# Performance work log

Measured on AMD Instinct MI355X. Metric: run time of the kernel, lower is better.

The kernel has to match this reference:

```python
import jax, jax.numpy as jnp
import numpy as np

INPUT_SIZE = 1024
HIDDEN_SIZE = 1024
BATCH = 32
SEQ_LEN = 1024


def setup_inputs() -> dict:
    key = jax.random.key(0)
    k1, k2, k3, k4 = jax.random.split(key, 4)
    scale_x = 1.0 / np.sqrt(INPUT_SIZE)
    scale_h = 1.0 / np.sqrt(HIDDEN_SIZE)
    X = jax.random.normal(k1, (BATCH, SEQ_LEN, INPUT_SIZE), dtype=jnp.float32)
    W_xh = jax.random.normal(k2, (INPUT_SIZE, HIDDEN_SIZE), dtype=jnp.float32) * scale_x
    W_hh = jax.random.normal(k3, (HIDDEN_SIZE, HIDDEN_SIZE), dtype=jnp.float32) * scale_h
    b_h = jax.random.normal(k4, (HIDDEN_SIZE,), dtype=jnp.float32) * 0.01
    return {"X": X, "W_xh": W_xh, "W_hh": W_hh, "b_h": b_h}


def reference(X, W_xh, W_hh, b_h):
    # Elman RNN: H_t = tanh(X_t @ W_xh + H_{t-1} @ W_hh + b)
    B, S, _ = X.shape
    H0 = jnp.zeros((B, W_hh.shape[0]), dtype=X.dtype)
    # Precompute input projection for all timesteps in one big GEMM.
    Xp = jnp.einsum('bsi,ih->bsh', X, W_xh) + b_h  # [B, S, H]

    def step(H, xp_t):
        H_new = jnp.tanh(xp_t + H @ W_hh)
        return H_new, H_new

    H_last, outs = jax.lax.scan(step, H0, jnp.swapaxes(Xp, 0, 1))  # outs: [S, B, H]
    out = jnp.swapaxes(outs, 0, 1)  # [B, S, H]
    return out, H_last
```

## Files before the change

kernel.cpp:

```cpp
#include <hip/hip_runtime.h>
#include <math.h>


#define B_SZ 32
#define S_SZ 1024
#define H_SZ 1024
#define K_SZ 1024

#define BM 128
#define BN 128
#define BK 8

__global__ __launch_bounds__(256) void proj_gemm(
    const float* __restrict__ A,
    const float* __restrict__ Bm,
    const float* __restrict__ bias,
    float* __restrict__ C,
    int M, int N, int K)
{
    __shared__ float As[BK][BM];
    __shared__ float Bs[BK][BN];

    const int tid  = threadIdx.x;
    const int row0 = blockIdx.y * BM;
    const int col0 = blockIdx.x * BN;
    const int tx = tid & 15;
    const int ty = tid >> 4;
    const int mBase = ty * 8;
    const int nBase = tx * 8;

    float acc[8][8];
    #pragma unroll
    for (int i = 0; i < 8; ++i)
        #pragma unroll
        for (int j = 0; j < 8; ++j) acc[i][j] = 0.f;

    for (int k0 = 0; k0 < K; k0 += BK) {
        {
            const int r  = tid >> 1;
            const int kq = (tid & 1) * 4;
            const float4 av = *(const float4*)(&A[(size_t)(row0 + r) * K + k0 + kq]);
            As[kq + 0][r] = av.x;
            As[kq + 1][r] = av.y;
            As[kq + 2][r] = av.z;
            As[kq + 3][r] = av.w;
            const int kr = tid >> 5;
            const int cq = (tid & 31) * 4;
            *(float4*)(&Bs[kr][cq]) =
                *(const float4*)(&Bm[(size_t)(k0 + kr) * N + col0 + cq]);
        }
        __syncthreads();

        #pragma unroll
        for (int kk = 0; kk < BK; ++kk) {
            float a[8], b[8];
            *(float4*)&a[0] = *(const float4*)&As[kk][mBase];
            *(float4*)&a[4] = *(const float4*)&As[kk][mBase + 4];
            *(float4*)&b[0] = *(const float4*)&Bs[kk][nBase];
            *(float4*)&b[4] = *(const float4*)&Bs[kk][nBase + 4];
            #pragma unroll
            for (int i = 0; i < 8; ++i)
                #pragma unroll
                for (int j = 0; j < 8; ++j)
                    acc[i][j] += a[i] * b[j];
        }
        __syncthreads();
    }

    #pragma unroll
    for (int i = 0; i < 8; ++i) {
        const int r = row0 + mBase + i;
        #pragma unroll
        for (int jq = 0; jq < 8; jq += 4) {
            const int c = col0 + nBase + jq;
            const float4 bv = *(const float4*)(&bias[c]);
            float4 o;
            o.x = acc[i][jq + 0] + bv.x;
            o.y = acc[i][jq + 1] + bv.y;
            o.z = acc[i][jq + 2] + bv.z;
            o.w = acc[i][jq + 3] + bv.w;
            *(float4*)(&C[(size_t)r * N + c]) = o;
        }
    }
}

__global__ void init_cnt(unsigned int* __restrict__ cnt, int n) {
    int i = blockIdx.x * 256 + threadIdx.x;
    if (i < n) cnt[i] = 0u;
}

__device__ __forceinline__ float fast_tanh(float x) {
    const float cx = fminf(fmaxf(x, -15.f), 15.f);
    const float e  = __expf(2.f * cx);
    return __fdividef(e - 1.f, e + 1.f);
}

__global__ __launch_bounds__(512, 2) void rnn_persist(
    float* __restrict__ HS,
    const float* __restrict__ W,
    float* __restrict__ Hlast,
    unsigned int* __restrict__ cnt
    )
{
    const int g    = blockIdx.x & 7;
    const int c    = blockIdx.x >> 3;
    const int col0 = c * 32;
    const int b0   = g * 4;
    const int tid  = threadIdx.x;
    const int j    = tid & 31;
    const int seg  = tid >> 5;

    __shared__ __align__(16) float Hs[4][1024];
    __shared__ float red[8][4][32];

    float w[64];
    {
        const float* wp = W + (size_t)(seg * 64) * H_SZ + col0 + j;
        #pragma unroll
        for (int i = 0; i < 64; ++i) w[i] = wp[(size_t)i * H_SZ];
        #pragma unroll
        for (int i = 0; i < 64; ++i) asm volatile("" : "+v"(w[i]));
    }

    unsigned int* flag = cnt + g * S_SZ;

    const int eb = tid >> 5;
    const int ej = tid & 31;

    for (int t = 0; t < S_SZ; ++t) {
        float xp = 0.f;
        size_t eidx = 0;
        if (tid < 128) {
            eidx = ((size_t)(b0 + eb) * S_SZ + t) * H_SZ + col0 + ej;
            xp = HS[eidx];
        }

        if (t > 0) {
            if (tid == 0) {
                while (__hip_atomic_load(flag + (t - 1), __ATOMIC_RELAXED,
                                         __HIP_MEMORY_SCOPE_AGENT) < 32u) {
                    __builtin_amdgcn_s_sleep(2);
                }
            }
            __syncthreads();

            #pragma unroll
            for (int ch = 0; ch < 4; ++ch) {
                const int f8 = tid + ch * 512;
                const int b  = f8 >> 9;
                const int qw = f8 & 511;
                const unsigned long long* src = (const unsigned long long*)
                    (&HS[((size_t)(b0 + b) * S_SZ + (t - 1)) * H_SZ]);
                const unsigned long long v8 = __hip_atomic_load(
                    &src[qw], __ATOMIC_RELAXED, __HIP_MEMORY_SCOPE_AGENT);
                *(unsigned long long*)(&Hs[b][qw * 2]) = v8;
            }
            __syncthreads();

            float acc[4];
            #pragma unroll
            for (int b = 0; b < 4; ++b) {
                const float4* hb = (const float4*)(&Hs[b][seg * 64]);
                float a = 0.f;
                #pragma unroll
                for (int q = 0; q < 16; ++q) {
                    const float4 h = hb[q];
                    a += h.x * w[4 * q + 0];
                    a += h.y * w[4 * q + 1];
                    a += h.z * w[4 * q + 2];
                    a += h.w * w[4 * q + 3];
                }
                acc[b] = a;
            }
            #pragma unroll
            for (int b = 0; b < 4; ++b) acc[b] += __shfl_xor(acc[b], 32);
            const int wv = tid >> 6;
            if ((tid & 63) < 32) {
                #pragma unroll
                for (int b = 0; b < 4; ++b) red[wv][b][j] = acc[b];
            }
            __syncthreads();
        }

        if (tid < 128) {
            float s = 0.f;
            if (t > 0) {
                #pragma unroll
                for (int wv2 = 0; wv2 < 8; ++wv2) s += red[wv2][eb][ej];
            }
            const float v = fast_tanh(xp + s);
            __hip_atomic_store(&HS[eidx], v, __ATOMIC_RELAXED,
                               __HIP_MEMORY_SCOPE_AGENT);
            if (t == S_SZ - 1)
                Hlast[(size_t)(b0 + eb) * H_SZ + col0 + ej] = v;
        }

        __syncthreads();
        if (tid == 0) {
            __hip_atomic_fetch_add(flag + t, 1u, __ATOMIC_RELAXED,
                                   __HIP_MEMORY_SCOPE_AGENT);
        }
    }
}

extern "C" void kernel_launch(void* const* d_in, const int* in_sizes, int n_in,
                              void* d_out, int out_size, void* d_ws, size_t ws_size,
                              hipStream_t stream) {
    const float* X    = (const float*)d_in[0];
    const float* W_xh = (const float*)d_in[1];
    const float* W_hh = (const float*)d_in[2];
    const float* b_h  = (const float*)d_in[3];
    float* out = (float*)d_out;
    float* Hlast = out + (size_t)B_SZ * S_SZ * H_SZ;
    unsigned int* cnt = (unsigned int*)d_ws;

    init_cnt<<<(8 * S_SZ + 255) / 256, 256, 0, stream>>>(cnt, 8 * S_SZ);

    dim3 gridA(H_SZ / BN, (B_SZ * S_SZ) / BM);
    proj_gemm<<<gridA, 256, 0, stream>>>(X, W_xh, b_h, out,
                                         B_SZ * S_SZ, H_SZ, K_SZ);

    rnn_persist<<<256, 512, 0, stream>>>(out, W_hh, Hlast, cnt);
}
```

Baseline: 4.248 ms.

## Replace counter flags with per-element tagged values in double-buffered exchange

Hidden-state values are published as 64-bit words packing the timestep tag with the float, in a two-slot parity buffer. Consumers poll each element directly until its tag matches, removing the single-thread flag spin, a block barrier and the per-step atomic counter increment. This cuts per-step synchronization latency on the sequential recurrence, at the cost of doubled exchange traffic and all threads spinning on global memory.

```diff
diff --git a/kernel.cpp b/kernel.cpp
--- a/kernel.cpp
+++ b/kernel.cpp
@@ -84,9 +84,9 @@
     }
 }
 
-__global__ void init_cnt(unsigned int* __restrict__ cnt, int n) {
+__global__ void init_hx(unsigned long long* __restrict__ hx, int n) {
     int i = blockIdx.x * 256 + threadIdx.x;
-    if (i < n) cnt[i] = 0u;
+    if (i < n) hx[i] = 0xFFFFFFFF00000000ULL;
 }
 
 __device__ __forceinline__ float fast_tanh(float x) {
@@ -99,7 +99,7 @@
     float* __restrict__ HS,
     const float* __restrict__ W,
     float* __restrict__ Hlast,
-    unsigned int* __restrict__ cnt
+    unsigned long long* __restrict__ Hx
     )
 {
     const int g    = blockIdx.x & 7;
@@ -122,7 +122,7 @@
         for (int i = 0; i < 64; ++i) asm volatile("" : "+v"(w[i]));
     }
 
-    unsigned int* flag = cnt + g * S_SZ;
+    const size_t PAR = (size_t)B_SZ * H_SZ;
 
     const int eb = tid >> 5;
     const int ej = tid & 31;
@@ -136,24 +136,30 @@
         }
 
         if (t > 0) {
-            if (tid == 0) {
-                while (__hip_atomic_load(flag + (t - 1), __ATOMIC_RELAXED,
-                                         __HIP_MEMORY_SCOPE_AGENT) < 32u) {
-                    __builtin_amdgcn_s_sleep(2);
+            const unsigned int want = (unsigned int)(t - 1);
+            const unsigned long long* hxr =
+                Hx + ((size_t)((t - 1) & 1)) * PAR + (size_t)b0 * H_SZ;
+
+            unsigned long long v[8];
+            #pragma unroll
+            for (int q = 0; q < 8; ++q) {
+                v[q] = __hip_atomic_load(hxr + tid + 512 * q,
+                                         __ATOMIC_RELAXED,
+                                         __HIP_MEMORY_SCOPE_AGENT);
+            }
+            #pragma unroll
+            for (int q = 0; q < 8; ++q) {
+                while ((unsigned int)(v[q] >> 32) != want) {
+                    v[q] = __hip_atomic_load(hxr + tid + 512 * q,
+                                             __ATOMIC_RELAXED,
+                                             __HIP_MEMORY_SCOPE_AGENT);
                 }
             }
-            __syncthreads();
-
-            #pragma unroll
-            for (int ch = 0; ch < 4; ++ch) {
-                const int f8 = tid + ch * 512;
-                const int b  = f8 >> 9;
-                const int qw = f8 & 511;
-                const unsigned long long* src = (const unsigned long long*)
-                    (&HS[((size_t)(b0 + b) * S_SZ + (t - 1)) * H_SZ]);
-                const unsigned long long v8 = __hip_atomic_load(
-                    &src[qw], __ATOMIC_RELAXED, __HIP_MEMORY_SCOPE_AGENT);
-                *(unsigned long long*)(&Hs[b][qw * 2]) = v8;
+            #pragma unroll
+            for (int q = 0; q < 8; ++q) {
+                const int e = tid + 512 * q;
+                Hs[e >> 10][e & 1023] =
+                    __uint_as_float((unsigned int)v[q]);
             }
             __syncthreads();
 
@@ -179,8 +185,8 @@
                 #pragma unroll
                 for (int b = 0; b < 4; ++b) red[wv][b][j] = acc[b];
             }
-            __syncthreads();
-        }
+        }
+        __syncthreads();
 
         if (tid < 128) {
             float s = 0.f;
@@ -189,16 +195,16 @@
                 for (int wv2 = 0; wv2 < 8; ++wv2) s += red[wv2][eb][ej];
             }
             const float v = fast_tanh(xp + s);
-            __hip_atomic_store(&HS[eidx], v, __ATOMIC_RELAXED,
-                               __HIP_MEMORY_SCOPE_AGENT);
+            HS[eidx] = v;
+            const unsigned long long pk =
+                ((unsigned long long)(unsigned int)t << 32) |
+                (unsigned long long)__float_as_uint(v);
+            __hip_atomic_store(
+                Hx + ((size_t)(t & 1)) * PAR +
+                    (size_t)(b0 + eb) * H_SZ + col0 + ej,
+                pk, __ATOMIC_RELAXED, __HIP_MEMORY_SCOPE_AGENT);
             if (t == S_SZ - 1)
                 Hlast[(size_t)(b0 + eb) * H_SZ + col0 + ej] = v;
-        }
-
-        __syncthreads();
-        if (tid == 0) {
-            __hip_atomic_fetch_add(flag + t, 1u, __ATOMIC_RELAXED,
-                                   __HIP_MEMORY_SCOPE_AGENT);
         }
     }
 }
@@ -212,13 +218,14 @@
     const float* b_h  = (const float*)d_in[3];
     float* out = (float*)d_out;
     float* Hlast = out + (size_t)B_SZ * S_SZ * H_SZ;
-    unsigned int* cnt = (unsigned int*)d_ws;
-
-    init_cnt<<<(8 * S_SZ + 255) / 256, 256, 0, stream>>>(cnt, 8 * S_SZ);
+    unsigned long long* Hx = (unsigned long long*)d_ws;
+
+    init_hx<<<(2 * B_SZ * H_SZ + 255) / 256, 256, 0, stream>>>(
+        Hx, 2 * B_SZ * H_SZ);
 
     dim3 gridA(H_SZ / BN, (B_SZ * S_SZ) / BM);
     proj_gemm<<<gridA, 256, 0, stream>>>(X, W_xh, b_h, out,
                                          B_SZ * S_SZ, H_SZ, K_SZ);
 
-    rnn_persist<<<256, 512, 0, stream>>>(out, W_hh, Hlast, cnt);
-}
+    rnn_persist<<<256, 512, 0, stream>>>(out, W_hh, Hlast, Hx);
+}
```

Measured after the change: 5.298 ms. 24.7% more time.
